# Performance work log

Hardware: AMD Instinct MI355X
Metric: run time of the kernel (lower is better)

Reference implementation:

```python
import jax, jax.numpy as jnp
import numpy as np

B, S, UNITS = 64, 2048, 1024


def setup_inputs() -> dict:
    key = jax.random.key(0)
    ks = jax.random.split(key, 6)
    scale = 1.0 / np.sqrt(UNITS)
    return {
        "s_prev": jax.random.normal(ks[0], (B, UNITS), dtype=jnp.float32),
        "hidden_states": jax.random.normal(ks[1], (B, S, UNITS), dtype=jnp.float32),
        "W_w": jax.random.normal(ks[2], (UNITS, UNITS), dtype=jnp.float32) * scale,
        "W_b": jnp.zeros((UNITS,), dtype=jnp.float32),
        "U_w": jax.random.normal(ks[3], (UNITS, UNITS), dtype=jnp.float32) * scale,
        "U_b": jnp.zeros((UNITS,), dtype=jnp.float32),
        "V_w": jax.random.normal(ks[4], (UNITS, 1), dtype=jnp.float32) * scale,
        "V_b": jnp.zeros((1,), dtype=jnp.float32),
    }


def reference(s_prev, hidden_states, W_w, W_b, U_w, U_b, V_w, V_b):
    # W(s_prev): [B, units] -> [B, 1, units]
    W_s = (s_prev @ W_w + W_b)[:, None, :]
    # U(hidden_states): [B, S, units]
    U_h = jnp.einsum('bsu,uk->bsk', hidden_states, U_w) + U_b
    # V(tanh(W_s + U_h)): [B, S, 1]
    scores = jnp.tanh(W_s + U_h) @ V_w + V_b
    # softmax over seq axis
    weights = jax.nn.softmax(scores, axis=1)  # [B, S, 1]
    # weighted sum over seq -> context [B, units]
    context = jnp.sum(weights * hidden_states, axis=1)
    return context, weights
```

## Files before the change

### kernel.cpp

```cpp
#include <hip/hip_runtime.h>

#define BB   64
#define SS   2048
#define UU   1024
#define MM   (BB * SS)

typedef unsigned short u16;
typedef unsigned int   u32;
typedef __attribute__((ext_vector_type(8))) short bf16x8;
typedef __attribute__((ext_vector_type(4))) float f32x4;

__device__ __forceinline__ u16 f2b(float f) {
    u32 x = __float_as_uint(f);
    u32 r = (x + 0x7fffu + ((x >> 16) & 1u)) >> 16;
    return (u16)r;
}
__device__ __forceinline__ float b2f(u16 u) {
    return __uint_as_float(((u32)u) << 16);
}
__device__ __forceinline__ float fast_tanh(float x) {
    x = fminf(fmaxf(x, -15.f), 15.f);
    float e = __expf(2.f * x);
    return (e - 1.f) / (e + 1.f);
}

__global__ __launch_bounds__(256) void k_transpose_uw(const float* __restrict__ Uw,
                                                      u16* __restrict__ UwT) {
    __shared__ float tile[64][65];
    int n0 = blockIdx.x * 64, k0 = blockIdx.y * 64;
    int c = threadIdx.x & 63, r0 = threadIdx.x >> 6;
#pragma unroll
    for (int i = 0; i < 64; i += 4)
        tile[r0 + i][c] = Uw[(size_t)(k0 + r0 + i) * UU + n0 + c];
    __syncthreads();
#pragma unroll
    for (int i = 0; i < 64; i += 4)
        UwT[(size_t)(n0 + r0 + i) * UU + k0 + c] = f2b(tile[c][r0 + i]);
}

__global__ __launch_bounds__(256) void k_convert_h(const float* __restrict__ src,
                                                   u16* __restrict__ dst) {
    size_t i = ((size_t)blockIdx.x * 256 + threadIdx.x) * 8;
    float4 f0 = *(const float4*)(src + i);
    float4 f1 = *(const float4*)(src + i + 4);
    u16 t[8];
    t[0] = f2b(f0.x); t[1] = f2b(f0.y); t[2] = f2b(f0.z); t[3] = f2b(f0.w);
    t[4] = f2b(f1.x); t[5] = f2b(f1.y); t[6] = f2b(f1.z); t[7] = f2b(f1.w);
    *(uint4*)(dst + i) = *(uint4*)t;
}

__global__ __launch_bounds__(256) void k_ws(const float* __restrict__ sp,
                                            const float* __restrict__ Ww,
                                            const float* __restrict__ Wb,
                                            float* __restrict__ Ws) {
    int u = blockIdx.x * 256 + threadIdx.x;
    int b = blockIdx.y;
    const float* sprow = sp + (size_t)b * UU;
    float acc = 0.f;
#pragma unroll 4
    for (int k = 0; k < UU; ++k)
        acc = fmaf(sprow[k], Ww[(size_t)k * UU + u], acc);
    Ws[(size_t)b * UU + u] = acc + Wb[u];
}

template <bool ABF16>
__global__ __launch_bounds__(256) void k_gemm(const void* __restrict__ Aptr,
                                              const u16* __restrict__ UwT,
                                              const float* __restrict__ Ws,
                                              const float* __restrict__ Ub,
                                              const float* __restrict__ Vw,
                                              float* __restrict__ scp) {
    __shared__ __align__(16) u16 As[128][72];
    __shared__ __align__(16) u16 Bs[128][72];
    const int tid  = threadIdx.x;
    const int lane = tid & 63;
    const int wave = tid >> 6;
    const int wm = wave >> 1, wn = wave & 1;
    const int quad = lane >> 4, l15 = lane & 15;
    const int nt = blockIdx.x;
    const int n0 = nt * 128;
    const size_t m0 = (size_t)blockIdx.y * 128;

    f32x4 acc[4][4];
#pragma unroll
    for (int i = 0; i < 4; ++i)
#pragma unroll
        for (int j = 0; j < 4; ++j) acc[i][j] = (f32x4){0.f, 0.f, 0.f, 0.f};

    const int sr = tid >> 3;
    const int sc = (tid & 7) * 8;

    for (int kk = 0; kk < UU; kk += 64) {
        if (ABF16) {
            const u16* A = (const u16*)Aptr;
#pragma unroll
            for (int i = 0; i < 4; ++i) {
                int r = sr + i * 32;
                uint4 v = *(const uint4*)(A + (m0 + r) * UU + kk + sc);
                *(uint4*)(&As[r][sc]) = v;
            }
        } else {
            const float* A = (const float*)Aptr;
#pragma unroll
            for (int i = 0; i < 4; ++i) {
                int r = sr + i * 32;
                const float4* p = (const float4*)(A + (m0 + r) * UU + kk + sc);
                float4 f0 = p[0], f1 = p[1];
                u16 t[8];
                t[0] = f2b(f0.x); t[1] = f2b(f0.y); t[2] = f2b(f0.z); t[3] = f2b(f0.w);
                t[4] = f2b(f1.x); t[5] = f2b(f1.y); t[6] = f2b(f1.z); t[7] = f2b(f1.w);
                *(uint4*)(&As[r][sc]) = *(uint4*)t;
            }
        }
#pragma unroll
        for (int i = 0; i < 4; ++i) {
            int r = sr + i * 32;
            uint4 v = *(const uint4*)(UwT + (size_t)(n0 + r) * UU + kk + sc);
            *(uint4*)(&Bs[r][sc]) = v;
        }
        __syncthreads();
#pragma unroll
        for (int k2 = 0; k2 < 64; k2 += 32) {
            bf16x8 a[4], b[4];
#pragma unroll
            for (int mi = 0; mi < 4; ++mi)
                a[mi] = *(const bf16x8*)(&As[wm * 64 + mi * 16 + l15][k2 + quad * 8]);
#pragma unroll
            for (int ni = 0; ni < 4; ++ni)
                b[ni] = *(const bf16x8*)(&Bs[wn * 64 + ni * 16 + l15][k2 + quad * 8]);
#pragma unroll
            for (int mi = 0; mi < 4; ++mi)
#pragma unroll
                for (int ni = 0; ni < 4; ++ni)
                    acc[mi][ni] = __builtin_amdgcn_mfma_f32_16x16x32_bf16(
                        a[mi], b[ni], acc[mi][ni], 0, 0, 0);
        }
        __syncthreads();
    }

    const int bidx = (int)(m0 >> 11);
    const float* wsrow = Ws + (size_t)bidx * UU;
    float wsv[4], ubv[4], vwv[4];
#pragma unroll
    for (int ni = 0; ni < 4; ++ni) {
        int ng = n0 + wn * 64 + ni * 16 + l15;
        wsv[ni] = wsrow[ng];
        ubv[ni] = Ub[ng];
        vwv[ni] = Vw[ng];
    }
#pragma unroll
    for (int mi = 0; mi < 4; ++mi) {
#pragma unroll
        for (int r = 0; r < 4; ++r) {
            float v = 0.f;
#pragma unroll
            for (int ni = 0; ni < 4; ++ni) {
                float x = acc[mi][ni][r] + wsv[ni] + ubv[ni];
                v = fmaf(fast_tanh(x), vwv[ni], v);
            }
#pragma unroll
            for (int off = 1; off < 16; off <<= 1)
                v += __shfl_xor(v, off, 64);
            if (l15 == 0) {
                size_t mg = m0 + wm * 64 + mi * 16 + quad * 4 + r;
                scp[mg * 16 + nt * 2 + wn] = v;
            }
        }
    }
}

__global__ __launch_bounds__(256) void k_softmax(const float* __restrict__ scp,
                                                 float* __restrict__ wout) {
    int b = blockIdx.x, t = threadIdx.x;
    __shared__ float red[256];
    float sc[8];
    float lmax = -1e30f;
#pragma unroll
    for (int i = 0; i < 8; ++i) {
        int s = t + i * 256;
        const float4* p = (const float4*)(scp + ((size_t)b * SS + s) * 16);
        float4 a = p[0], c = p[1], d = p[2], e = p[3];
        float v = (a.x + a.y + a.z + a.w) + (c.x + c.y + c.z + c.w) +
                  (d.x + d.y + d.z + d.w) + (e.x + e.y + e.z + e.w);
        sc[i] = v;
        lmax = fmaxf(lmax, v);
    }
    red[t] = lmax;
    __syncthreads();
    for (int o = 128; o > 0; o >>= 1) {
        if (t < o) red[t] = fmaxf(red[t], red[t + o]);
        __syncthreads();
    }
    float mx = red[0];
    __syncthreads();
    float lsum = 0.f;
#pragma unroll
    for (int i = 0; i < 8; ++i) {
        sc[i] = __expf(sc[i] - mx);
        lsum += sc[i];
    }
    red[t] = lsum;
    __syncthreads();
    for (int o = 128; o > 0; o >>= 1) {
        if (t < o) red[t] += red[t + o];
        __syncthreads();
    }
    float inv = 1.f / red[0];
#pragma unroll
    for (int i = 0; i < 8; ++i)
        wout[(size_t)b * SS + t + i * 256] = sc[i] * inv;
}

template <bool HBF16>
__global__ __launch_bounds__(256) void k_context(const void* __restrict__ hptr,
                                                 const float* __restrict__ w,
                                                 float* __restrict__ ctx) {
    int b = blockIdx.y;
    int s0 = blockIdx.x * 256;
    int u = threadIdx.x * 4;
    const float* wrow = w + (size_t)b * SS + s0;
    float a0 = 0.f, a1 = 0.f, a2 = 0.f, a3 = 0.f;
    for (int i = 0; i < 256; ++i) {
        float wv = wrow[i];
        size_t base = ((size_t)b * SS + s0 + i) * UU + u;
        if (HBF16) {
            ushort4 hv = *(const ushort4*)((const u16*)hptr + base);
            a0 = fmaf(wv, b2f(hv.x), a0);
            a1 = fmaf(wv, b2f(hv.y), a1);
            a2 = fmaf(wv, b2f(hv.z), a2);
            a3 = fmaf(wv, b2f(hv.w), a3);
        } else {
            float4 hv = *(const float4*)((const float*)hptr + base);
            a0 = fmaf(wv, hv.x, a0);
            a1 = fmaf(wv, hv.y, a1);
            a2 = fmaf(wv, hv.z, a2);
            a3 = fmaf(wv, hv.w, a3);
        }
    }
    atomicAdd(&ctx[(size_t)b * UU + u + 0], a0);
    atomicAdd(&ctx[(size_t)b * UU + u + 1], a1);
    atomicAdd(&ctx[(size_t)b * UU + u + 2], a2);
    atomicAdd(&ctx[(size_t)b * UU + u + 3], a3);
}

extern "C" void kernel_launch(void* const* d_in, const int* in_sizes, int n_in,
                              void* d_out, int out_size, void* d_ws, size_t ws_size,
                              hipStream_t stream) {
    const float* s_prev = (const float*)d_in[0];
    const float* h      = (const float*)d_in[1];
    const float* Ww     = (const float*)d_in[2];
    const float* Wb     = (const float*)d_in[3];
    const float* Uw     = (const float*)d_in[4];
    const float* Ub     = (const float*)d_in[5];
    const float* Vw     = (const float*)d_in[6];

    float* out = (float*)d_out;
    char* ws = (char*)d_ws;

    u16*   UwT = (u16*)ws;
    float* Ws  = (float*)(ws + (size_t)(2 << 20));
    float* scp = (float*)(ws + (size_t)(2 << 20) + (256 << 10));
    size_t offH = (size_t)(2 << 20) + (256 << 10) + ((size_t)8 << 20);
    u16*   hbf = (u16*)(ws + offH);
    const size_t hBytes = (size_t)MM * UU * 2;
    const bool useBf16 = (ws_size >= offH + hBytes);

    hipMemsetAsync(out, 0, (size_t)BB * UU * sizeof(float), stream);

    k_transpose_uw<<<dim3(16, 16), 256, 0, stream>>>(Uw, UwT);
    k_ws<<<dim3(4, BB), 256, 0, stream>>>(s_prev, Ww, Wb, Ws);

    if (useBf16) {
        k_convert_h<<<(MM * (UU / 8)) / 256, 256, 0, stream>>>(h, hbf);
        k_gemm<true><<<dim3(8, MM / 128), 256, 0, stream>>>(hbf, UwT, Ws, Ub, Vw, scp);
    } else {
        k_gemm<false><<<dim3(8, MM / 128), 256, 0, stream>>>(h, UwT, Ws, Ub, Vw, scp);
    }

    k_softmax<<<BB, 256, 0, stream>>>(scp, out + (size_t)BB * UU);

    if (useBf16)
        k_context<true><<<dim3(8, BB), 256, 0, stream>>>(hbf, out + (size_t)BB * UU, out);
    else
        k_context<false><<<dim3(8, BB), 256, 0, stream>>>(h, out + (size_t)BB * UU, out);
}
```

Measured before the change: 1.373 ms.

## Use direct global-to-LDS loads with XOR swizzle and grouped tile order in GEMM

The bf16 GEMM now loads A and B tiles straight into LDS with global_load_lds, using an XOR-swizzled layout in place of the padded layout. Blocks are remapped into groups so that neighbouring blocks share the A and B tiles in L2. The W·s_prev matvec is split along K into four blocks that combine their partial sums with atomics, and the context kernel doubles its grid to get more parallelism. The goals are fewer register round trips and better cache reuse, at the cost of extra atomics and a memset.

Result: faster. 1.262 ms (-8.1%).

```diff
diff --git a/kernel.cpp b/kernel.cpp
--- a/kernel.cpp
+++ b/kernel.cpp
@@ -22,6 +22,11 @@
     x = fminf(fmaxf(x, -15.f), 15.f);
     float e = __expf(2.f * x);
     return (e - 1.f) / (e + 1.f);
+}
+__device__ __forceinline__ void async_copy16(const u16* gp, u16* lp) {
+    __builtin_amdgcn_global_load_lds(
+        (const __attribute__((address_space(1))) unsigned int*)gp,
+        (__attribute__((address_space(3))) unsigned int*)lp, 16, 0, 0);
 }
 
 __global__ __launch_bounds__(256) void k_transpose_uw(const float* __restrict__ Uw,
@@ -55,21 +60,120 @@
                                             float* __restrict__ Ws) {
     int u = blockIdx.x * 256 + threadIdx.x;
     int b = blockIdx.y;
-    const float* sprow = sp + (size_t)b * UU;
-    float acc = 0.f;
+    int k0 = blockIdx.z * 256;
+    const float* sprow = sp + (size_t)b * UU + k0;
+    float acc = (blockIdx.z == 0) ? Wb[u] : 0.f;
 #pragma unroll 4
-    for (int k = 0; k < UU; ++k)
-        acc = fmaf(sprow[k], Ww[(size_t)k * UU + u], acc);
-    Ws[(size_t)b * UU + u] = acc + Wb[u];
-}
-
-template <bool ABF16>
-__global__ __launch_bounds__(256) void k_gemm(const void* __restrict__ Aptr,
-                                              const u16* __restrict__ UwT,
-                                              const float* __restrict__ Ws,
-                                              const float* __restrict__ Ub,
-                                              const float* __restrict__ Vw,
-                                              float* __restrict__ scp) {
+    for (int k = 0; k < 256; ++k)
+        acc = fmaf(sprow[k], Ww[(size_t)(k0 + k) * UU + u], acc);
+    atomicAdd(&Ws[(size_t)b * UU + u], acc);
+}
+
+__global__ __launch_bounds__(256) void k_gemm_lds(const u16* __restrict__ A,
+                                                  const u16* __restrict__ UwT,
+                                                  const float* __restrict__ Ws,
+                                                  const float* __restrict__ Ub,
+                                                  const float* __restrict__ Vw,
+                                                  float* __restrict__ scp) {
+    __shared__ __align__(16) u16 As[128 * 64];
+    __shared__ __align__(16) u16 Bs[128 * 64];
+    const int tid  = threadIdx.x;
+    const int lane = tid & 63;
+    const int wave = tid >> 6;
+    const int wm = wave >> 1, wn = wave & 1;
+    const int quad = lane >> 4, l15 = lane & 15;
+
+    const int bid = blockIdx.x;
+    const int g   = bid >> 6;
+    const int mt  = g * 8 + (bid & 7);
+    const int nt  = (bid >> 3) & 7;
+    const int n0  = nt * 128;
+    const size_t m0 = (size_t)mt * 128;
+
+    const int srow   = lane >> 3;
+    const int schunk = (lane & 7) ^ srow;
+    const size_t lane_off = (size_t)srow * UU + (size_t)schunk * 8;
+
+    f32x4 acc[4][4];
+#pragma unroll
+    for (int i = 0; i < 4; ++i)
+#pragma unroll
+        for (int j = 0; j < 4; ++j) acc[i][j] = (f32x4){0.f, 0.f, 0.f, 0.f};
+
+    for (int kk = 0; kk < UU; kk += 64) {
+#pragma unroll
+        for (int i = 0; i < 4; ++i) {
+            const int gi = wave * 4 + i;
+            async_copy16(A + (m0 + gi * 8) * UU + kk + lane_off, As + gi * 512);
+        }
+#pragma unroll
+        for (int i = 0; i < 4; ++i) {
+            const int gi = wave * 4 + i;
+            async_copy16(UwT + (size_t)(n0 + gi * 8) * UU + kk + lane_off, Bs + gi * 512);
+        }
+        __syncthreads();
+#pragma unroll
+        for (int k2 = 0; k2 < 2; ++k2) {
+            const int chunk = quad + k2 * 4;
+            const int pos = chunk ^ (l15 & 7);
+            bf16x8 a[4], b[4];
+#pragma unroll
+            for (int mi = 0; mi < 4; ++mi) {
+                int r = wm * 64 + mi * 16 + l15;
+                a[mi] = *(const bf16x8*)(As + r * 64 + pos * 8);
+            }
+#pragma unroll
+            for (int ni = 0; ni < 4; ++ni) {
+                int r = wn * 64 + ni * 16 + l15;
+                b[ni] = *(const bf16x8*)(Bs + r * 64 + pos * 8);
+            }
+#pragma unroll
+            for (int mi = 0; mi < 4; ++mi)
+#pragma unroll
+                for (int ni = 0; ni < 4; ++ni)
+                    acc[mi][ni] = __builtin_amdgcn_mfma_f32_16x16x32_bf16(
+                        a[mi], b[ni], acc[mi][ni], 0, 0, 0);
+        }
+        __syncthreads();
+    }
+
+    const int bidx = (int)(m0 >> 11);
+    const float* wsrow = Ws + (size_t)bidx * UU;
+    float wsv[4], ubv[4], vwv[4];
+#pragma unroll
+    for (int ni = 0; ni < 4; ++ni) {
+        int ng = n0 + wn * 64 + ni * 16 + l15;
+        wsv[ni] = wsrow[ng];
+        ubv[ni] = Ub[ng];
+        vwv[ni] = Vw[ng];
+    }
+#pragma unroll
+    for (int mi = 0; mi < 4; ++mi) {
+#pragma unroll
+        for (int r = 0; r < 4; ++r) {
+            float v = 0.f;
+#pragma unroll
+            for (int ni = 0; ni < 4; ++ni) {
+                float x = acc[mi][ni][r] + wsv[ni] + ubv[ni];
+                v = fmaf(fast_tanh(x), vwv[ni], v);
+            }
+#pragma unroll
+            for (int off = 1; off < 16; off <<= 1)
+                v += __shfl_xor(v, off, 64);
+            if (l15 == 0) {
+                size_t mg = m0 + wm * 64 + mi * 16 + quad * 4 + r;
+                scp[mg * 16 + nt * 2 + wn] = v;
+            }
+        }
+    }
+}
+
+__global__ __launch_bounds__(256) void k_gemm_f32(const float* __restrict__ Aptr,
+                                                  const u16* __restrict__ UwT,
+                                                  const float* __restrict__ Ws,
+                                                  const float* __restrict__ Ub,
+                                                  const float* __restrict__ Vw,
+                                                  float* __restrict__ scp) {
     __shared__ __align__(16) u16 As[128][72];
     __shared__ __align__(16) u16 Bs[128][72];
     const int tid  = threadIdx.x;
@@ -91,26 +195,15 @@
     const int sc = (tid & 7) * 8;
 
     for (int kk = 0; kk < UU; kk += 64) {
-        if (ABF16) {
-            const u16* A = (const u16*)Aptr;
-#pragma unroll
-            for (int i = 0; i < 4; ++i) {
-                int r = sr + i * 32;
-                uint4 v = *(const uint4*)(A + (m0 + r) * UU + kk + sc);
-                *(uint4*)(&As[r][sc]) = v;
-            }
-        } else {
-            const float* A = (const float*)Aptr;
-#pragma unroll
-            for (int i = 0; i < 4; ++i) {
-                int r = sr + i * 32;
-                const float4* p = (const float4*)(A + (m0 + r) * UU + kk + sc);
-                float4 f0 = p[0], f1 = p[1];
-                u16 t[8];
-                t[0] = f2b(f0.x); t[1] = f2b(f0.y); t[2] = f2b(f0.z); t[3] = f2b(f0.w);
-                t[4] = f2b(f1.x); t[5] = f2b(f1.y); t[6] = f2b(f1.z); t[7] = f2b(f1.w);
-                *(uint4*)(&As[r][sc]) = *(uint4*)t;
-            }
+#pragma unroll
+        for (int i = 0; i < 4; ++i) {
+            int r = sr + i * 32;
+            const float4* p = (const float4*)(Aptr + (m0 + r) * UU + kk + sc);
+            float4 f0 = p[0], f1 = p[1];
+            u16 t[8];
+            t[0] = f2b(f0.x); t[1] = f2b(f0.y); t[2] = f2b(f0.z); t[3] = f2b(f0.w);
+            t[4] = f2b(f1.x); t[5] = f2b(f1.y); t[6] = f2b(f1.z); t[7] = f2b(f1.w);
+            *(uint4*)(&As[r][sc]) = *(uint4*)t;
         }
 #pragma unroll
         for (int i = 0; i < 4; ++i) {
@@ -216,11 +309,11 @@
                                                  const float* __restrict__ w,
                                                  float* __restrict__ ctx) {
     int b = blockIdx.y;
-    int s0 = blockIdx.x * 256;
+    int s0 = blockIdx.x * 128;
     int u = threadIdx.x * 4;
     const float* wrow = w + (size_t)b * SS + s0;
     float a0 = 0.f, a1 = 0.f, a2 = 0.f, a3 = 0.f;
-    for (int i = 0; i < 256; ++i) {
+    for (int i = 0; i < 128; ++i) {
         float wv = wrow[i];
         size_t base = ((size_t)b * SS + s0 + i) * UU + u;
         if (HBF16) {
@@ -266,21 +359,22 @@
     const bool useBf16 = (ws_size >= offH + hBytes);
 
     hipMemsetAsync(out, 0, (size_t)BB * UU * sizeof(float), stream);
+    hipMemsetAsync(Ws, 0, (size_t)BB * UU * sizeof(float), stream);
 
     k_transpose_uw<<<dim3(16, 16), 256, 0, stream>>>(Uw, UwT);
-    k_ws<<<dim3(4, BB), 256, 0, stream>>>(s_prev, Ww, Wb, Ws);
+    k_ws<<<dim3(4, BB, 4), 256, 0, stream>>>(s_prev, Ww, Wb, Ws);
 
     if (useBf16) {
         k_convert_h<<<(MM * (UU / 8)) / 256, 256, 0, stream>>>(h, hbf);
-        k_gemm<true><<<dim3(8, MM / 128), 256, 0, stream>>>(hbf, UwT, Ws, Ub, Vw, scp);
+        k_gemm_lds<<<8192, 256, 0, stream>>>(hbf, UwT, Ws, Ub, Vw, scp);
     } else {
-        k_gemm<false><<<dim3(8, MM / 128), 256, 0, stream>>>(h, UwT, Ws, Ub, Vw, scp);
+        k_gemm_f32<<<dim3(8, MM / 128), 256, 0, stream>>>(h, UwT, Ws, Ub, Vw, scp);
     }
 
     k_softmax<<<BB, 256, 0, stream>>>(scp, out + (size_t)BB * UU);
 
     if (useBf16)
-        k_context<true><<<dim3(8, BB), 256, 0, stream>>>(hbf, out + (size_t)BB * UU, out);
+        k_context<true><<<dim3(16, BB), 256, 0, stream>>>(hbf, out + (size_t)BB * UU, out);
     else
-        k_context<false><<<dim3(8, BB), 256, 0, stream>>>(h, out + (size_t)BB * UU, out);
-}
+        k_context<false><<<dim3(16, BB), 256, 0, stream>>>(h, out + (size_t)BB * UU, out);
+}
```
